# Kernel tuning notes

Measured on AMD Instinct MI355X. Metric: run time of the kernel, lower is better.

Reference implementation:

```python
import math
import jax, jax.numpy as jnp
import numpy as np

HEADS = 16
MODEL = 1024
KEY = 64
VAL = 64
B, S = 4, 2048


def setup_inputs() -> dict:
    key = jax.random.key(0)
    ks = jax.random.split(key, 8)
    queries = jax.random.normal(ks[0], (B, S, MODEL), dtype=jnp.float32)
    keys_ = jax.random.normal(ks[1], (B, S, MODEL), dtype=jnp.float32)
    values = jax.random.normal(ks[2], (B, S, MODEL), dtype=jnp.float32)
    # causal boolean mask, true = attention allowed (every row has >=1 True)
    masks = jnp.broadcast_to(jnp.tril(jnp.ones((S, S), dtype=bool)), (B, S, S))
    lim_in = 1.0 / math.sqrt(MODEL)
    # stacked per-head projection weights, stored as [H, model, head_dim]
    Wq = jax.random.uniform(ks[3], (HEADS, MODEL, KEY), minval=-lim_in, maxval=lim_in, dtype=jnp.float32)
    Wk = jax.random.uniform(ks[4], (HEADS, MODEL, KEY), minval=-lim_in, maxval=lim_in, dtype=jnp.float32)
    Wv = jax.random.uniform(ks[5], (HEADS, MODEL, VAL), minval=-lim_in, maxval=lim_in, dtype=jnp.float32)
    lim_o = 1.0 / math.sqrt(HEADS * VAL)
    Wo = jax.random.uniform(ks[6], (HEADS * VAL, MODEL), minval=-lim_o, maxval=lim_o, dtype=jnp.float32)
    bo = jax.random.uniform(ks[7], (MODEL,), minval=-lim_o, maxval=lim_o, dtype=jnp.float32)
    return {"queries": queries, "keys": keys_, "values": values, "masks": masks,
            "Wq": Wq, "Wk": Wk, "Wv": Wv, "Wo": Wo, "bo": bo}


def reference(queries, keys, values, masks, Wq, Wk, Wv, Wo, bo):
    # per-head projections, batched over heads: [B,S,M] x [H,M,D] -> [B,H,S,D]
    q = jnp.einsum('bsm,hmd->bhsd', queries, Wq)
    k = jnp.einsum('bsm,hmd->bhsd', keys, Wk)
    v = jnp.einsum('bsm,hmd->bhsd', values, Wv)
    scale = 1.0 / math.sqrt(KEY)
    scores = jnp.einsum('bhqd,bhkd->bhqk', q, k) * scale  # [B,H,Q,K]
    scores = jnp.where(masks[:, None, :, :], scores, -jnp.inf)
    weights = jax.nn.softmax(scores, axis=-1)
    out = jnp.einsum('bhqk,bhkv->bhqv', weights, v)  # [B,H,Q,V]
    # concat heads along feature dim (head-major order matches torch concat)
    out = out.transpose(0, 2, 1, 3).reshape(B, S, HEADS * VAL)
    return out @ Wo + bo
```

## Files before the change

### kernel.cpp

```cpp
#include <hip/hip_runtime.h>


typedef __bf16 bf16;
typedef __attribute__((ext_vector_type(8))) __bf16 bf16x8;
typedef __attribute__((ext_vector_type(4))) __bf16 bf16x4;
typedef __attribute__((ext_vector_type(4))) float f32x4;
typedef unsigned int u32;

#define GLB_AS __attribute__((address_space(1)))
#define LDS_AS __attribute__((address_space(3)))

#define L2E 1.44269504088896340736f

static __device__ __forceinline__ void stage_swz(const bf16* __restrict__ g, long ldelem,
                                                 long row0, long col0,
                                                 bf16* lds, int rows, int tid)
{
    const int lane = tid & 63;
    const int wave = tid >> 6;
    const int nch = rows >> 3;
    for (int c = wave; c < nch; c += 4) {
        unsigned o  = ((unsigned)c << 10) + ((unsigned)lane << 4);
        unsigned r  = o >> 7;
        unsigned cb = o & 127u;
        unsigned cs = cb ^ ((r & 7u) << 4);
        const bf16* src = g + (row0 + (long)r) * ldelem + col0 + (long)(cs >> 1);
        char* dst = (char*)lds + ((unsigned)c << 10);
        __builtin_amdgcn_global_load_lds((GLB_AS u32*)src, (LDS_AS u32*)dst, 16, 0, 0);
    }
}

__global__ void cast3(const float4* __restrict__ a, const float4* __restrict__ b,
                      const float4* __restrict__ c,
                      bf16x4* __restrict__ xa, bf16x4* __restrict__ xb,
                      bf16x4* __restrict__ xc)
{
    const int n4 = (8192 * 1024) / 4;
    for (int i = blockIdx.x * blockDim.x + threadIdx.x; i < n4; i += gridDim.x * blockDim.x) {
        float4 v;
        v = a[i]; xa[i] = (bf16x4){(bf16)v.x, (bf16)v.y, (bf16)v.z, (bf16)v.w};
        v = b[i]; xb[i] = (bf16x4){(bf16)v.x, (bf16)v.y, (bf16)v.z, (bf16)v.w};
        v = c[i]; xc[i] = (bf16x4){(bf16)v.x, (bf16)v.y, (bf16)v.z, (bf16)v.w};
    }
}

__global__ void transw3(const float* __restrict__ wq, const float* __restrict__ wk,
                        const float* __restrict__ wv, const float* __restrict__ wo,
                        bf16* __restrict__ wqT, bf16* __restrict__ wkT,
                        bf16* __restrict__ wvT, bf16* __restrict__ woT)
{
    const int n = 16 * 1024 * 64;
    for (int i = blockIdx.x * blockDim.x + threadIdx.x; i < n; i += gridDim.x * blockDim.x) {
        int h = i >> 16, m = (i >> 6) & 1023, d = i & 63;
        long t = ((long)((h << 6) + d) << 10) + m;
        wqT[t] = (bf16)(wq[i] * 0.125f);
        wkT[t] = (bf16)wk[i];
        wvT[t] = (bf16)wv[i];
        int f = i >> 10, nn = i & 1023;
        woT[((long)nn << 10) + f] = (bf16)wo[i];
    }
}

template<int MODE>
__global__ __launch_bounds__(256, 2) void gemm8k(const bf16* __restrict__ A,
                                                 const bf16* __restrict__ Bt,
                                                 bf16* __restrict__ Cb,
                                                 float* __restrict__ Cf,
                                                 const float* __restrict__ bias)
{
    __shared__ alignas(16) bf16 sA[128 * 64];
    __shared__ alignas(16) bf16 sB[128 * 64];
    const int tid = threadIdx.x, lane = tid & 63, wave = tid >> 6;
    const int wr = wave >> 1, wc = wave & 1;
    const long row0 = (long)blockIdx.x << 7;
    const long col0 = (long)blockIdx.y << 7;

    f32x4 acc[4][4];
#pragma unroll
    for (int i = 0; i < 4; ++i)
#pragma unroll
        for (int j = 0; j < 4; ++j) acc[i][j] = (f32x4){0.f, 0.f, 0.f, 0.f};

    for (int kt = 0; kt < 16; ++kt) {
        __syncthreads();
        stage_swz(A,  1024, row0, (long)kt << 6, sA, 128, tid);
        stage_swz(Bt, 1024, col0, (long)kt << 6, sB, 128, tid);
        __syncthreads();
#pragma unroll
        for (int kk = 0; kk < 2; ++kk) {
            bf16x8 af[4], bfr[4];
            const unsigned kb = (unsigned)(kk << 6) + (unsigned)((lane >> 4) << 4);
#pragma unroll
            for (int i = 0; i < 4; ++i) {
                unsigned r = (unsigned)((wr << 6) + (i << 4) + (lane & 15));
                af[i] = *(const bf16x8*)((const char*)sA + (r << 7) + (kb ^ ((r & 7u) << 4)));
            }
#pragma unroll
            for (int j = 0; j < 4; ++j) {
                unsigned r = (unsigned)((wc << 6) + (j << 4) + (lane & 15));
                bfr[j] = *(const bf16x8*)((const char*)sB + (r << 7) + (kb ^ ((r & 7u) << 4)));
            }
#pragma unroll
            for (int i = 0; i < 4; ++i)
#pragma unroll
                for (int j = 0; j < 4; ++j)
                    acc[i][j] = __builtin_amdgcn_mfma_f32_16x16x32_bf16(af[i], bfr[j], acc[i][j], 0, 0, 0);
        }
    }

#pragma unroll
    for (int i = 0; i < 4; ++i) {
#pragma unroll
        for (int j = 0; j < 4; ++j) {
#pragma unroll
            for (int rr = 0; rr < 4; ++rr) {
                long row = row0 + (wr << 6) + (i << 4) + ((lane >> 4) << 2) + rr;
                long col = col0 + (wc << 6) + (j << 4) + (lane & 15);
                float v = acc[i][j][rr];
                if constexpr (MODE == 2) {
                    Cf[row * 1024 + col] = v + bias[col];
                } else if constexpr (MODE == 0) {
                    long idx = (((row >> 11) << 4) + (col >> 6)) * 131072 + (row & 2047) * 64 + (col & 63);
                    Cb[idx] = (bf16)v;
                } else {
                    long idx = (((row >> 11) << 4) + (col >> 6)) * 131072 + (col & 63) * 2048 + (row & 2047);
                    Cb[idx] = (bf16)v;
                }
            }
        }
    }
}

__global__ __launch_bounds__(256, 2) void attn(const bf16* __restrict__ q,
                                               const bf16* __restrict__ k,
                                               const bf16* __restrict__ vT,
                                               bf16* __restrict__ o)
{
    __shared__ alignas(16) bf16 sK[2][64 * 64];
    __shared__ alignas(16) bf16 sV[2][64 * 64];
    __shared__ alignas(16) bf16 sP[4][32 * 72];
    const int tid = threadIdx.x, lane = tid & 63, wave = tid >> 6;
    const int h = blockIdx.y, b = blockIdx.z;
    const long hb = (long)(b * 16 + h);
    const bf16* qh = q  + hb * 131072;
    const bf16* kh = k  + hb * 131072;
    const bf16* vh = vT + hb * 131072;

    for (int half = 0; half < 2; ++half) {
        const int qt = half ? (15 - (int)blockIdx.x) : (int)blockIdx.x;
        const int qw = (qt << 7) + (wave << 5);

        bf16x8 aq[2][2];
#pragma unroll
        for (int mf = 0; mf < 2; ++mf)
#pragma unroll
            for (int kk = 0; kk < 2; ++kk)
                aq[mf][kk] = *(const bf16x8*)(qh + (long)(qw + (mf << 4) + (lane & 15)) * 64
                                                 + (kk << 5) + ((lane >> 4) << 3));

        f32x4 accO[2][4];
        float mrow[2][4], lrow[2][4];
#pragma unroll
        for (int mf = 0; mf < 2; ++mf) {
#pragma unroll
            for (int nf = 0; nf < 4; ++nf) accO[mf][nf] = (f32x4){0.f, 0.f, 0.f, 0.f};
#pragma unroll
            for (int rr = 0; rr < 4; ++rr) { mrow[mf][rr] = -1e30f; lrow[mf][rr] = 0.f; }
        }

        const int nkv = (qt << 1) + 2;
        __syncthreads();
        stage_swz(kh, 64,   0, 0, sK[0], 64, tid);
        stage_swz(vh, 2048, 0, 0, sV[0], 64, tid);

        for (int kvt = 0; kvt < nkv; ++kvt) {
            const int cur = kvt & 1;
            const int kv0 = kvt << 6;
            __syncthreads();
            if (kvt + 1 < nkv) {
                stage_swz(kh, 64,   (long)(kv0 + 64), 0, sK[cur ^ 1], 64, tid);
                stage_swz(vh, 2048, 0, (long)(kv0 + 64), sV[cur ^ 1], 64, tid);
            }
            if (kv0 > qw + 31) continue;

            f32x4 s[2][4];
#pragma unroll
            for (int mf = 0; mf < 2; ++mf)
#pragma unroll
                for (int nf = 0; nf < 4; ++nf) s[mf][nf] = (f32x4){0.f, 0.f, 0.f, 0.f};
#pragma unroll
            for (int kk = 0; kk < 2; ++kk) {
                bf16x8 bk[4];
                const unsigned kb = (unsigned)(kk << 6) + (unsigned)((lane >> 4) << 4);
#pragma unroll
                for (int nf = 0; nf < 4; ++nf) {
                    unsigned r = (unsigned)((nf << 4) + (lane & 15));
                    bk[nf] = *(const bf16x8*)((const char*)sK[cur] + (r << 7) + (kb ^ ((r & 7u) << 4)));
                }
#pragma unroll
                for (int mf = 0; mf < 2; ++mf)
#pragma unroll
                    for (int nf = 0; nf < 4; ++nf)
                        s[mf][nf] = __builtin_amdgcn_mfma_f32_16x16x32_bf16(aq[mf][kk], bk[nf], s[mf][nf], 0, 0, 0);
            }

            if (kv0 + 63 > qw) {
#pragma unroll
                for (int mf = 0; mf < 2; ++mf)
#pragma unroll
                    for (int rr = 0; rr < 4; ++rr) {
                        const int ra = qw + (mf << 4) + ((lane >> 4) << 2) + rr;
#pragma unroll
                        for (int nf = 0; nf < 4; ++nf)
                            if ((kv0 + (nf << 4) + (lane & 15)) > ra) s[mf][nf][rr] = -1e30f;
                    }
            }

#pragma unroll
            for (int mf = 0; mf < 2; ++mf) {
#pragma unroll
                for (int rr = 0; rr < 4; ++rr) {
                    float mt = fmaxf(fmaxf(s[mf][0][rr], s[mf][1][rr]), fmaxf(s[mf][2][rr], s[mf][3][rr]));
                    mt = fmaxf(mt, __shfl_xor(mt, 1));
                    mt = fmaxf(mt, __shfl_xor(mt, 2));
                    mt = fmaxf(mt, __shfl_xor(mt, 4));
                    mt = fmaxf(mt, __shfl_xor(mt, 8));
                    if (mt > mrow[mf][rr]) {
                        const float cf = __builtin_exp2f((mrow[mf][rr] - mt) * L2E);
                        mrow[mf][rr] = mt;
                        lrow[mf][rr] *= cf;
#pragma unroll
                        for (int nf = 0; nf < 4; ++nf) accO[mf][nf][rr] *= cf;
                    }
                    const float mnew = mrow[mf][rr];
                    float rs = 0.f;
#pragma unroll
                    for (int nf = 0; nf < 4; ++nf) {
                        float p = __builtin_exp2f((s[mf][nf][rr] - mnew) * L2E);
                        s[mf][nf][rr] = p;
                        rs += p;
                    }
                    rs += __shfl_xor(rs, 1);
                    rs += __shfl_xor(rs, 2);
                    rs += __shfl_xor(rs, 4);
                    rs += __shfl_xor(rs, 8);
                    lrow[mf][rr] += rs;
                }
            }

            bf16* pw = &sP[wave][0];
#pragma unroll
            for (int mf = 0; mf < 2; ++mf)
#pragma unroll
                for (int nf = 0; nf < 4; ++nf)
#pragma unroll
                    for (int rr = 0; rr < 4; ++rr)
                        pw[((mf << 4) + ((lane >> 4) << 2) + rr) * 72 + (nf << 4) + (lane & 15)] =
                            (bf16)s[mf][nf][rr];

#pragma unroll
            for (int kk = 0; kk < 2; ++kk) {
                bf16x8 pa[2], bv[4];
#pragma unroll
                for (int mf = 0; mf < 2; ++mf)
                    pa[mf] = *(const bf16x8*)(pw + ((mf << 4) + (lane & 15)) * 72
                                                 + (kk << 5) + ((lane >> 4) << 3));
                const unsigned kb = (unsigned)(kk << 6) + (unsigned)((lane >> 4) << 4);
#pragma unroll
                for (int nf = 0; nf < 4; ++nf) {
                    unsigned r = (unsigned)((nf << 4) + (lane & 15));
                    bv[nf] = *(const bf16x8*)((const char*)sV[cur] + (r << 7) + (kb ^ ((r & 7u) << 4)));
                }
#pragma unroll
                for (int mf = 0; mf < 2; ++mf)
#pragma unroll
                    for (int nf = 0; nf < 4; ++nf)
                        accO[mf][nf] = __builtin_amdgcn_mfma_f32_16x16x32_bf16(pa[mf], bv[nf], accO[mf][nf], 0, 0, 0);
            }
        }

#pragma unroll
        for (int mf = 0; mf < 2; ++mf)
#pragma unroll
            for (int rr = 0; rr < 4; ++rr) {
                const float inv = 1.f / lrow[mf][rr];
                const long ra = qw + (mf << 4) + ((lane >> 4) << 2) + rr;
#pragma unroll
                for (int nf = 0; nf < 4; ++nf)
                    o[((long)b * 2048 + ra) * 1024 + (h << 6) + (nf << 4) + (lane & 15)] =
                        (bf16)(accO[mf][nf][rr] * inv);
            }
    }
}

extern "C" void kernel_launch(void* const* d_in, const int* in_sizes, int n_in,
                              void* d_out, int out_size, void* d_ws, size_t ws_size,
                              hipStream_t stream)
{
    const float* queries = (const float*)d_in[0];
    const float* keys    = (const float*)d_in[1];
    const float* values  = (const float*)d_in[2];
    const float* Wq = (const float*)d_in[4];
    const float* Wk = (const float*)d_in[5];
    const float* Wv = (const float*)d_in[6];
    const float* Wo = (const float*)d_in[7];
    const float* bo = (const float*)d_in[8];
    float* out = (float*)d_out;

    bf16* Xq  = (bf16*)d_ws;
    bf16* Xk  = Xq  + 8388608;
    bf16* Xv  = Xk  + 8388608;
    bf16* WqT = Xv  + 8388608;
    bf16* WkT = WqT + 1048576;
    bf16* WvT = WkT + 1048576;
    bf16* WoT = WvT + 1048576;
    bf16* qp  = WoT + 1048576;
    bf16* kp  = qp  + 8388608;
    bf16* vTp = Xq;
    bf16* ao  = Xk;
    if (ws_size < (size_t)92274688) return;

    cast3<<<dim3(2048), dim3(256), 0, stream>>>((const float4*)queries, (const float4*)keys,
                                                (const float4*)values,
                                                (bf16x4*)Xq, (bf16x4*)Xk, (bf16x4*)Xv);
    transw3<<<dim3(1024), dim3(256), 0, stream>>>(Wq, Wk, Wv, Wo, WqT, WkT, WvT, WoT);
    gemm8k<0><<<dim3(64, 8), dim3(256), 0, stream>>>(Xq, WqT, qp,  nullptr, nullptr);
    gemm8k<0><<<dim3(64, 8), dim3(256), 0, stream>>>(Xk, WkT, kp,  nullptr, nullptr);
    gemm8k<1><<<dim3(64, 8), dim3(256), 0, stream>>>(Xv, WvT, vTp, nullptr, nullptr);
    attn<<<dim3(8, 16, 4), dim3(256), 0, stream>>>(qp, kp, vTp, ao);
    gemm8k<2><<<dim3(64, 8), dim3(256), 0, stream>>>(ao, WoT, nullptr, out, bo);
}
```

Measured before the change: 450.6 us.

## Double-buffer GEMM staging, tile weight transposes, restructure attention grid and row sums

Double-buffers the GEMM's LDS tiles so the next k-tile load overlaps the current MFMA work. Replaces the scattered per-element weight transpose with a shared-memory tiled transpose. The attention kernel now runs one q-tile per block on a flat 1024-block grid, heaviest tiles first, with occupancy hinted at 3. It also computes softmax row sums with an extra MFMA against a ones vector instead of shuffle reductions. The GEMM LDS footprint doubles and the extra MFMA adds matrix work, but the GEMM's barrier before compute is removed; the async-load wait then relies on the loop-top barrier.

After: 468.3 us. +3.9%, slower.

```diff
diff --git a/kernel.cpp b/kernel.cpp
--- a/kernel.cpp
+++ b/kernel.cpp
@@ -44,20 +44,37 @@
     }
 }
 
-__global__ void transw3(const float* __restrict__ wq, const float* __restrict__ wk,
-                        const float* __restrict__ wv, const float* __restrict__ wo,
-                        bf16* __restrict__ wqT, bf16* __restrict__ wkT,
-                        bf16* __restrict__ wvT, bf16* __restrict__ woT)
-{
-    const int n = 16 * 1024 * 64;
-    for (int i = blockIdx.x * blockDim.x + threadIdx.x; i < n; i += gridDim.x * blockDim.x) {
-        int h = i >> 16, m = (i >> 6) & 1023, d = i & 63;
-        long t = ((long)((h << 6) + d) << 10) + m;
-        wqT[t] = (bf16)(wq[i] * 0.125f);
-        wkT[t] = (bf16)wk[i];
-        wvT[t] = (bf16)wv[i];
-        int f = i >> 10, nn = i & 1023;
-        woT[((long)nn << 10) + f] = (bf16)wo[i];
+__global__ void transw(const float* __restrict__ wq, const float* __restrict__ wk,
+                       const float* __restrict__ wv, const float* __restrict__ wo,
+                       bf16* __restrict__ wqT, bf16* __restrict__ wkT,
+                       bf16* __restrict__ wvT, bf16* __restrict__ woT)
+{
+    __shared__ float t[64][65];
+    const int tid = threadIdx.x, bx = blockIdx.x, by = blockIdx.y;
+    const float* srcs[3] = {wq, wk, wv};
+    bf16* dsts[3] = {wqT, wkT, wvT};
+#pragma unroll
+    for (int m = 0; m < 3; ++m) {
+        const float sc = (m == 0) ? 0.125f : 1.0f;
+        for (int i = tid; i < 4096; i += 256) {
+            int r = i >> 6, c = i & 63;
+            t[c][r] = srcs[m][by * 65536 + (bx * 64 + r) * 64 + c];
+        }
+        __syncthreads();
+        for (int i = tid; i < 4096; i += 256) {
+            int r = i >> 6, c = i & 63;
+            dsts[m][(long)(by * 64 + r) * 1024 + bx * 64 + c] = (bf16)(t[r][c] * sc);
+        }
+        __syncthreads();
+    }
+    for (int i = tid; i < 4096; i += 256) {
+        int r = i >> 6, c = i & 63;
+        t[c][r] = wo[(long)(bx * 64 + r) * 1024 + by * 64 + c];
+    }
+    __syncthreads();
+    for (int i = tid; i < 4096; i += 256) {
+        int r = i >> 6, c = i & 63;
+        woT[(long)(by * 64 + r) * 1024 + bx * 64 + c] = (bf16)t[r][c];
     }
 }
 
@@ -68,8 +85,8 @@
                                                  float* __restrict__ Cf,
                                                  const float* __restrict__ bias)
 {
-    __shared__ alignas(16) bf16 sA[128 * 64];
-    __shared__ alignas(16) bf16 sB[128 * 64];
+    __shared__ alignas(16) bf16 sA[2][128 * 64];
+    __shared__ alignas(16) bf16 sB[2][128 * 64];
     const int tid = threadIdx.x, lane = tid & 63, wave = tid >> 6;
     const int wr = wave >> 1, wc = wave & 1;
     const long row0 = (long)blockIdx.x << 7;
@@ -81,11 +98,16 @@
 #pragma unroll
         for (int j = 0; j < 4; ++j) acc[i][j] = (f32x4){0.f, 0.f, 0.f, 0.f};
 
+    stage_swz(A,  1024, row0, 0, sA[0], 128, tid);
+    stage_swz(Bt, 1024, col0, 0, sB[0], 128, tid);
+
     for (int kt = 0; kt < 16; ++kt) {
+        const int cur = kt & 1;
         __syncthreads();
-        stage_swz(A,  1024, row0, (long)kt << 6, sA, 128, tid);
-        stage_swz(Bt, 1024, col0, (long)kt << 6, sB, 128, tid);
-        __syncthreads();
+        if (kt + 1 < 16) {
+            stage_swz(A,  1024, row0, (long)(kt + 1) << 6, sA[cur ^ 1], 128, tid);
+            stage_swz(Bt, 1024, col0, (long)(kt + 1) << 6, sB[cur ^ 1], 128, tid);
+        }
 #pragma unroll
         for (int kk = 0; kk < 2; ++kk) {
             bf16x8 af[4], bfr[4];
@@ -93,12 +115,12 @@
 #pragma unroll
             for (int i = 0; i < 4; ++i) {
                 unsigned r = (unsigned)((wr << 6) + (i << 4) + (lane & 15));
-                af[i] = *(const bf16x8*)((const char*)sA + (r << 7) + (kb ^ ((r & 7u) << 4)));
+                af[i] = *(const bf16x8*)((const char*)sA[cur] + (r << 7) + (kb ^ ((r & 7u) << 4)));
             }
 #pragma unroll
             for (int j = 0; j < 4; ++j) {
                 unsigned r = (unsigned)((wc << 6) + (j << 4) + (lane & 15));
-                bfr[j] = *(const bf16x8*)((const char*)sB + (r << 7) + (kb ^ ((r & 7u) << 4)));
+                bfr[j] = *(const bf16x8*)((const char*)sB[cur] + (r << 7) + (kb ^ ((r & 7u) << 4)));
             }
 #pragma unroll
             for (int i = 0; i < 4; ++i)
@@ -131,7 +153,7 @@
     }
 }
 
-__global__ __launch_bounds__(256, 2) void attn(const bf16* __restrict__ q,
+__global__ __launch_bounds__(256, 3) void attn(const bf16* __restrict__ q,
                                                const bf16* __restrict__ k,
                                                const bf16* __restrict__ vT,
                                                bf16* __restrict__ o)
@@ -140,157 +162,152 @@
     __shared__ alignas(16) bf16 sV[2][64 * 64];
     __shared__ alignas(16) bf16 sP[4][32 * 72];
     const int tid = threadIdx.x, lane = tid & 63, wave = tid >> 6;
-    const int h = blockIdx.y, b = blockIdx.z;
-    const long hb = (long)(b * 16 + h);
-    const bf16* qh = q  + hb * 131072;
-    const bf16* kh = k  + hb * 131072;
-    const bf16* vh = vT + hb * 131072;
-
-    for (int half = 0; half < 2; ++half) {
-        const int qt = half ? (15 - (int)blockIdx.x) : (int)blockIdx.x;
-        const int qw = (qt << 7) + (wave << 5);
-
-        bf16x8 aq[2][2];
+    const int bid = blockIdx.x;
+    const int swz = ((bid & 7) << 7) + (bid >> 3);
+    const int qt = 15 - (swz & 15);
+    const int hb = swz >> 4;
+    const int h = hb & 15, b = hb >> 4;
+    const bf16* qh = q  + (long)hb * 131072;
+    const bf16* kh = k  + (long)hb * 131072;
+    const bf16* vh = vT + (long)hb * 131072;
+    const int qw = (qt << 7) + (wave << 5);
+
+    bf16x8 aq[2][2];
+#pragma unroll
+    for (int mf = 0; mf < 2; ++mf)
+#pragma unroll
+        for (int kk = 0; kk < 2; ++kk)
+            aq[mf][kk] = *(const bf16x8*)(qh + (long)(qw + (mf << 4) + (lane & 15)) * 64
+                                             + (kk << 5) + ((lane >> 4) << 3));
+    bf16x8 vone;
+#pragma unroll
+    for (int i = 0; i < 8; ++i) vone[i] = (bf16)1.0f;
+
+    f32x4 accO[2][4], accOl[2];
+    float mrow[2][4];
+#pragma unroll
+    for (int mf = 0; mf < 2; ++mf) {
+#pragma unroll
+        for (int nf = 0; nf < 4; ++nf) accO[mf][nf] = (f32x4){0.f, 0.f, 0.f, 0.f};
+        accOl[mf] = (f32x4){0.f, 0.f, 0.f, 0.f};
+#pragma unroll
+        for (int rr = 0; rr < 4; ++rr) mrow[mf][rr] = -1e30f;
+    }
+
+    const int nkv = (qt << 1) + 2;
+    stage_swz(kh, 64,   0, 0, sK[0], 64, tid);
+    stage_swz(vh, 2048, 0, 0, sV[0], 64, tid);
+
+    for (int kvt = 0; kvt < nkv; ++kvt) {
+        const int cur = kvt & 1;
+        const int kv0 = kvt << 6;
+        __syncthreads();
+        if (kvt + 1 < nkv) {
+            stage_swz(kh, 64,   (long)(kv0 + 64), 0, sK[cur ^ 1], 64, tid);
+            stage_swz(vh, 2048, 0, (long)(kv0 + 64), sV[cur ^ 1], 64, tid);
+        }
+        if (kv0 > qw + 31) continue;
+
+        f32x4 s[2][4];
 #pragma unroll
         for (int mf = 0; mf < 2; ++mf)
 #pragma unroll
-            for (int kk = 0; kk < 2; ++kk)
-                aq[mf][kk] = *(const bf16x8*)(qh + (long)(qw + (mf << 4) + (lane & 15)) * 64
-                                                 + (kk << 5) + ((lane >> 4) << 3));
-
-        f32x4 accO[2][4];
-        float mrow[2][4], lrow[2][4];
+            for (int nf = 0; nf < 4; ++nf) s[mf][nf] = (f32x4){0.f, 0.f, 0.f, 0.f};
+#pragma unroll
+        for (int kk = 0; kk < 2; ++kk) {
+            bf16x8 bk[4];
+            const unsigned kb = (unsigned)(kk << 6) + (unsigned)((lane >> 4) << 4);
+#pragma unroll
+            for (int nf = 0; nf < 4; ++nf) {
+                unsigned r = (unsigned)((nf << 4) + (lane & 15));
+                bk[nf] = *(const bf16x8*)((const char*)sK[cur] + (r << 7) + (kb ^ ((r & 7u) << 4)));
+            }
+#pragma unroll
+            for (int mf = 0; mf < 2; ++mf)
+#pragma unroll
+                for (int nf = 0; nf < 4; ++nf)
+                    s[mf][nf] = __builtin_amdgcn_mfma_f32_16x16x32_bf16(aq[mf][kk], bk[nf], s[mf][nf], 0, 0, 0);
+        }
+
+        if (kv0 + 63 > qw) {
+#pragma unroll
+            for (int mf = 0; mf < 2; ++mf)
+#pragma unroll
+                for (int rr = 0; rr < 4; ++rr) {
+                    const int ra = qw + (mf << 4) + ((lane >> 4) << 2) + rr;
+#pragma unroll
+                    for (int nf = 0; nf < 4; ++nf)
+                        if ((kv0 + (nf << 4) + (lane & 15)) > ra) s[mf][nf][rr] = -1e30f;
+                }
+        }
+
 #pragma unroll
         for (int mf = 0; mf < 2; ++mf) {
 #pragma unroll
-            for (int nf = 0; nf < 4; ++nf) accO[mf][nf] = (f32x4){0.f, 0.f, 0.f, 0.f};
-#pragma unroll
-            for (int rr = 0; rr < 4; ++rr) { mrow[mf][rr] = -1e30f; lrow[mf][rr] = 0.f; }
-        }
-
-        const int nkv = (qt << 1) + 2;
-        __syncthreads();
-        stage_swz(kh, 64,   0, 0, sK[0], 64, tid);
-        stage_swz(vh, 2048, 0, 0, sV[0], 64, tid);
-
-        for (int kvt = 0; kvt < nkv; ++kvt) {
-            const int cur = kvt & 1;
-            const int kv0 = kvt << 6;
-            __syncthreads();
-            if (kvt + 1 < nkv) {
-                stage_swz(kh, 64,   (long)(kv0 + 64), 0, sK[cur ^ 1], 64, tid);
-                stage_swz(vh, 2048, 0, (long)(kv0 + 64), sV[cur ^ 1], 64, tid);
-            }
-            if (kv0 > qw + 31) continue;
-
-            f32x4 s[2][4];
+            for (int rr = 0; rr < 4; ++rr) {
+                float mt = fmaxf(fmaxf(s[mf][0][rr], s[mf][1][rr]), fmaxf(s[mf][2][rr], s[mf][3][rr]));
+                mt = fmaxf(mt, __shfl_xor(mt, 1));
+                mt = fmaxf(mt, __shfl_xor(mt, 2));
+                mt = fmaxf(mt, __shfl_xor(mt, 4));
+                mt = fmaxf(mt, __shfl_xor(mt, 8));
+                if (mt > mrow[mf][rr]) {
+                    const float cf = __builtin_exp2f((mrow[mf][rr] - mt) * L2E);
+                    mrow[mf][rr] = mt;
+                    accOl[mf][rr] *= cf;
+#pragma unroll
+                    for (int nf = 0; nf < 4; ++nf) accO[mf][nf][rr] *= cf;
+                }
+                const float m2 = mrow[mf][rr] * L2E;
+#pragma unroll
+                for (int nf = 0; nf < 4; ++nf)
+                    s[mf][nf][rr] = __builtin_exp2f(__builtin_fmaf(s[mf][nf][rr], L2E, -m2));
+            }
+        }
+
+        bf16* pw = &sP[wave][0];
+#pragma unroll
+        for (int mf = 0; mf < 2; ++mf)
+#pragma unroll
+            for (int nf = 0; nf < 4; ++nf)
+#pragma unroll
+                for (int rr = 0; rr < 4; ++rr)
+                    pw[((mf << 4) + ((lane >> 4) << 2) + rr) * 72 + (nf << 4) + (lane & 15)] =
+                        (bf16)s[mf][nf][rr];
+
+#pragma unroll
+        for (int kk = 0; kk < 2; ++kk) {
+            bf16x8 pa[2], bv[4];
 #pragma unroll
             for (int mf = 0; mf < 2; ++mf)
-#pragma unroll
-                for (int nf = 0; nf < 4; ++nf) s[mf][nf] = (f32x4){0.f, 0.f, 0.f, 0.f};
-#pragma unroll
-            for (int kk = 0; kk < 2; ++kk) {
-                bf16x8 bk[4];
-                const unsigned kb = (unsigned)(kk << 6) + (unsigned)((lane >> 4) << 4);
-#pragma unroll
-                for (int nf = 0; nf < 4; ++nf) {
-                    unsigned r = (unsigned)((nf << 4) + (lane & 15));
-                    bk[nf] = *(const bf16x8*)((const char*)sK[cur] + (r << 7) + (kb ^ ((r & 7u) << 4)));
-                }
-#pragma unroll
-                for (int mf = 0; mf < 2; ++mf)
-#pragma unroll
-                    for (int nf = 0; nf < 4; ++nf)
-                        s[mf][nf] = __builtin_amdgcn_mfma_f32_16x16x32_bf16(aq[mf][kk], bk[nf], s[mf][nf], 0, 0, 0);
-            }
-
-            if (kv0 + 63 > qw) {
-#pragma unroll
-                for (int mf = 0; mf < 2; ++mf)
-#pragma unroll
-                    for (int rr = 0; rr < 4; ++rr) {
-                        const int ra = qw + (mf << 4) + ((lane >> 4) << 2) + rr;
-#pragma unroll
-                        for (int nf = 0; nf < 4; ++nf)
-                            if ((kv0 + (nf << 4) + (lane & 15)) > ra) s[mf][nf][rr] = -1e30f;
-                    }
-            }
-
+                pa[mf] = *(const bf16x8*)(pw + ((mf << 4) + (lane & 15)) * 72
+                                             + (kk << 5) + ((lane >> 4) << 3));
+            const unsigned kb = (unsigned)(kk << 6) + (unsigned)((lane >> 4) << 4);
+#pragma unroll
+            for (int nf = 0; nf < 4; ++nf) {
+                unsigned r = (unsigned)((nf << 4) + (lane & 15));
+                bv[nf] = *(const bf16x8*)((const char*)sV[cur] + (r << 7) + (kb ^ ((r & 7u) << 4)));
+            }
 #pragma unroll
             for (int mf = 0; mf < 2; ++mf) {
 #pragma unroll
-                for (int rr = 0; rr < 4; ++rr) {
-                    float mt = fmaxf(fmaxf(s[mf][0][rr], s[mf][1][rr]), fmaxf(s[mf][2][rr], s[mf][3][rr]));
-                    mt = fmaxf(mt, __shfl_xor(mt, 1));
-                    mt = fmaxf(mt, __shfl_xor(mt, 2));
-                    mt = fmaxf(mt, __shfl_xor(mt, 4));
-                    mt = fmaxf(mt, __shfl_xor(mt, 8));
-                    if (mt > mrow[mf][rr]) {
-                        const float cf = __builtin_exp2f((mrow[mf][rr] - mt) * L2E);
-                        mrow[mf][rr] = mt;
-                        lrow[mf][rr] *= cf;
-#pragma unroll
-                        for (int nf = 0; nf < 4; ++nf) accO[mf][nf][rr] *= cf;
-                    }
-                    const float mnew = mrow[mf][rr];
-                    float rs = 0.f;
-#pragma unroll
-                    for (int nf = 0; nf < 4; ++nf) {
-                        float p = __builtin_exp2f((s[mf][nf][rr] - mnew) * L2E);
-                        s[mf][nf][rr] = p;
-                        rs += p;
-                    }
-                    rs += __shfl_xor(rs, 1);
-                    rs += __shfl_xor(rs, 2);
-                    rs += __shfl_xor(rs, 4);
-                    rs += __shfl_xor(rs, 8);
-                    lrow[mf][rr] += rs;
-                }
-            }
-
-            bf16* pw = &sP[wave][0];
-#pragma unroll
-            for (int mf = 0; mf < 2; ++mf)
-#pragma unroll
                 for (int nf = 0; nf < 4; ++nf)
-#pragma unroll
-                    for (int rr = 0; rr < 4; ++rr)
-                        pw[((mf << 4) + ((lane >> 4) << 2) + rr) * 72 + (nf << 4) + (lane & 15)] =
-                            (bf16)s[mf][nf][rr];
-
-#pragma unroll
-            for (int kk = 0; kk < 2; ++kk) {
-                bf16x8 pa[2], bv[4];
-#pragma unroll
-                for (int mf = 0; mf < 2; ++mf)
-                    pa[mf] = *(const bf16x8*)(pw + ((mf << 4) + (lane & 15)) * 72
-                                                 + (kk << 5) + ((lane >> 4) << 3));
-                const unsigned kb = (unsigned)(kk << 6) + (unsigned)((lane >> 4) << 4);
-#pragma unroll
-                for (int nf = 0; nf < 4; ++nf) {
-                    unsigned r = (unsigned)((nf << 4) + (lane & 15));
-                    bv[nf] = *(const bf16x8*)((const char*)sV[cur] + (r << 7) + (kb ^ ((r & 7u) << 4)));
-                }
-#pragma unroll
-                for (int mf = 0; mf < 2; ++mf)
-#pragma unroll
-                    for (int nf = 0; nf < 4; ++nf)
-                        accO[mf][nf] = __builtin_amdgcn_mfma_f32_16x16x32_bf16(pa[mf], bv[nf], accO[mf][nf], 0, 0, 0);
-            }
-        }
-
-#pragma unroll
-        for (int mf = 0; mf < 2; ++mf)
-#pragma unroll
-            for (int rr = 0; rr < 4; ++rr) {
-                const float inv = 1.f / lrow[mf][rr];
-                const long ra = qw + (mf << 4) + ((lane >> 4) << 2) + rr;
-#pragma unroll
-                for (int nf = 0; nf < 4; ++nf)
-                    o[((long)b * 2048 + ra) * 1024 + (h << 6) + (nf << 4) + (lane & 15)] =
-                        (bf16)(accO[mf][nf][rr] * inv);
-            }
-    }
+                    accO[mf][nf] = __builtin_amdgcn_mfma_f32_16x16x32_bf16(pa[mf], bv[nf], accO[mf][nf], 0, 0, 0);
+                accOl[mf] = __builtin_amdgcn_mfma_f32_16x16x32_bf16(pa[mf], vone, accOl[mf], 0, 0, 0);
+            }
+        }
+    }
+
+#pragma unroll
+    for (int mf = 0; mf < 2; ++mf)
+#pragma unroll
+        for (int rr = 0; rr < 4; ++rr) {
+            const float inv = 1.f / accOl[mf][rr];
+            const long ra = qw + (mf << 4) + ((lane >> 4) << 2) + rr;
+#pragma unroll
+            for (int nf = 0; nf < 4; ++nf)
+                o[((long)b * 2048 + ra) * 1024 + (h << 6) + (nf << 4) + (lane & 15)] =
+                    (bf16)(accO[mf][nf][rr] * inv);
+        }
 }
 
 extern "C" void kernel_launch(void* const* d_in, const int* in_sizes, int n_in,
@@ -323,10 +340,10 @@
     cast3<<<dim3(2048), dim3(256), 0, stream>>>((const float4*)queries, (const float4*)keys,
                                                 (const float4*)values,
                                                 (bf16x4*)Xq, (bf16x4*)Xk, (bf16x4*)Xv);
-    transw3<<<dim3(1024), dim3(256), 0, stream>>>(Wq, Wk, Wv, Wo, WqT, WkT, WvT, WoT);
+    transw<<<dim3(16, 16), dim3(256), 0, stream>>>(Wq, Wk, Wv, Wo, WqT, WkT, WvT, WoT);
     gemm8k<0><<<dim3(64, 8), dim3(256), 0, stream>>>(Xq, WqT, qp,  nullptr, nullptr);
     gemm8k<0><<<dim3(64, 8), dim3(256), 0, stream>>>(Xk, WkT, kp,  nullptr, nullptr);
     gemm8k<1><<<dim3(64, 8), dim3(256), 0, stream>>>(Xv, WvT, vTp, nullptr, nullptr);
-    attn<<<dim3(8, 16, 4), dim3(256), 0, stream>>>(qp, kp, vTp, ao);
+    attn<<<dim3(1024), dim3(256), 0, stream>>>(qp, kp, vTp, ao);
     gemm8k<2><<<dim3(64, 8), dim3(256), 0, stream>>>(ao, WoT, nullptr, out, bo);
 }
```
